# Kernel tuning notes

Hardware: AMD Instinct MI355X
Metric: run time of the kernel (lower is better)

## Reference

```python
import jax, jax.numpy as jnp
import numpy as np

FEATURE_IN = 4096
FEATURE_OUT = 4096
R = 16
ALPHA = 32.0


def setup_inputs() -> dict:
    key = jax.random.key(0)
    k_x, k_w, k_b, k_a = jax.random.split(key, 4)
    x = jax.random.normal(k_x, (4, 2048, FEATURE_IN), dtype=jnp.float32)
    # base linear (torch nn.Linear): weight [out, in], bias [out]
    bound = 1.0 / np.sqrt(FEATURE_IN)
    w = jax.random.uniform(k_w, (FEATURE_OUT, FEATURE_IN), dtype=jnp.float32, minval=-bound, maxval=bound)
    b = jax.random.uniform(k_b, (FEATURE_OUT,), dtype=jnp.float32, minval=-bound, maxval=bound)
    # lora_a: kaiming uniform over [feature_in, r]; lora_b: zeros -> use small randn so grads are nontrivial? No: faithful init is zeros, but zeros makes LoRA path trivially zero. Use kaiming for a, small random for b to exercise the math.
    gain = np.sqrt(2.0 / (1.0 + 5.0 ** 2))  # kaiming_uniform default a=sqrt(5)
    bound_a = gain * np.sqrt(3.0 / FEATURE_IN)
    lora_a = jax.random.uniform(k_a, (FEATURE_IN, R), dtype=jnp.float32, minval=-bound_a, maxval=bound_a)
    lora_b = jax.random.normal(jax.random.fold_in(key, 7), (R, FEATURE_OUT), dtype=jnp.float32) * 0.01
    return {"x": x, "w": w, "b": b, "lora_a": lora_a, "lora_b": lora_b}


def reference(x, w, b, lora_a, lora_b):
    # base linear: x @ W^T + b
    output1 = jnp.einsum('bsi,oi->bso', x, w) + b
    # faithful to source: materialize (A @ B) [feature_in, feature_out] first,
    # then x @ (A@B), scaled by alpha/r
    ab = jnp.matmul(lora_a, lora_b)  # [feature_in, feature_out]
    output2 = jnp.matmul(x, ab) * (ALPHA / R)
    return output2 + output1
```

## Files before the change

### kernel.cpp

```cpp
#include <hip/hip_runtime.h>
#include <cstdint>
#include <cstddef>

#define FEATURE_IN 4096
#define FEATURE_OUT 4096
#define RNK 16

typedef __bf16 bf16x8_t __attribute__((ext_vector_type(8)));
typedef __bf16 bf16x4_t __attribute__((ext_vector_type(4)));
typedef float f32x4_t __attribute__((ext_vector_type(4)));

#define FW_KB 128
#define FW_NB 32
#define NFUSE 4096
#define NCVTB 2048
#define CVT_THREADS (NCVTB * 256)
#define CVT_CHUNKS 16

__global__ __launch_bounds__(256) void prep_all(const float* __restrict__ x,
                                                uint16_t* __restrict__ xb,
                                                const float* __restrict__ w,
                                                const float* __restrict__ la,
                                                const float* __restrict__ lb,
                                                uint16_t* __restrict__ wf) {
    __shared__ float las[FW_KB * RNK];
    __shared__ float lbs[RNK * FW_NB];

    const int tid = threadIdx.x;

    if (blockIdx.x >= NFUSE) {
        const int tg = (blockIdx.x - NFUSE) * 256 + tid;
        const f32x4_t* xp = (const f32x4_t*)x;
        bf16x4_t* op = (bf16x4_t*)xb;
#pragma unroll
        for (int i = 0; i < CVT_CHUNKS; ++i) {
            const int idx = i * CVT_THREADS + tg;
            f32x4_t v = xp[idx];
            bf16x4_t o;
            o[0] = (__bf16)v[0]; o[1] = (__bf16)v[1];
            o[2] = (__bf16)v[2]; o[3] = (__bf16)v[3];
            op[idx] = o;
        }
        return;
    }

    const int bid = blockIdx.x;
    const int kb = (bid & 31) * FW_KB;
    const int nb = (bid >> 5) * FW_NB;

    {
        const float4* src = (const float4*)(la + (size_t)kb * RNK);
        float4* dst = (float4*)las;
        dst[tid] = src[tid];
        dst[tid + 256] = src[tid + 256];
    }
#pragma unroll
    for (int f = tid; f < RNK * FW_NB; f += 256) {
        int r = f >> 5;
        int nl = f & 31;
        lbs[r * FW_NB + nl] = lb[(size_t)r * FEATURE_OUT + nb + nl];
    }
    __syncthreads();

    const int nl = tid >> 3;
    const int kq = tid & 7;

    f32x4_t bcol[4];
#pragma unroll
    for (int r4 = 0; r4 < 4; ++r4) {
        f32x4_t v;
#pragma unroll
        for (int j = 0; j < 4; ++j) v[j] = lbs[(r4 * 4 + j) * FW_NB + nl];
        bcol[r4] = v;
    }

    const f32x4_t* las4 = (const f32x4_t*)las;
    const float* wrow = w + (size_t)(nb + nl) * FEATURE_IN + kb + kq * 16;
    uint16_t* wfrow = wf + (size_t)(nb + nl) * FEATURE_IN + kb + kq * 16;

#pragma unroll
    for (int h = 0; h < 2; ++h) {
        float4 wv0 = ((const float4*)wrow)[h * 2 + 0];
        float4 wv1 = ((const float4*)wrow)[h * 2 + 1];
        float wfv[8] = {wv0.x, wv0.y, wv0.z, wv0.w, wv1.x, wv1.y, wv1.z, wv1.w};
        bf16x8_t o;
#pragma unroll
        for (int j = 0; j < 8; ++j) {
            const int k = kq * 16 + h * 8 + j;
            float s = 0.f;
#pragma unroll
            for (int rr = 0; rr < 4; ++rr) {
                const int r4 = (rr + kq) & 3;
                f32x4_t av = las4[k * 4 + r4];
                f32x4_t bv = bcol[r4];
                s += av[0] * bv[0] + av[1] * bv[1] + av[2] * bv[2] + av[3] * bv[3];
            }
            o[j] = (__bf16)(wfv[j] + 2.f * s);
        }
        ((bf16x8_t*)wfrow)[h] = o;
    }
}

#define BM 256
#define BN 256
#define BK 32
#define NT (FEATURE_IN / BK)

#define ABUF(b) ((b) * 32768)
#define BBUF(b) ((b) * 32768 + 16384)

#define MFMA16X(S) do { _Pragma("unroll")                                                \
    for (int _mi = 0; _mi < 4; ++_mi) { _Pragma("unroll")                                \
        for (int _ni = 0; _ni < 4; ++_ni)                                                \
            acc[_mi][_ni] = __builtin_amdgcn_mfma_f32_16x16x32_bf16(                     \
                afx[S][_mi], bqr[S][_ni], acc[_mi][_ni], 0, 0, 0); } } while (0)

#define MFMA16Y(S) do { _Pragma("unroll")                                                \
    for (int _mi = 0; _mi < 4; ++_mi) { _Pragma("unroll")                                \
        for (int _ni = 0; _ni < 4; ++_ni)                                                \
            acc[4 + _mi][_ni] = __builtin_amdgcn_mfma_f32_16x16x32_bf16(                 \
                afy[_mi], bqr[S][_ni], acc[4 + _mi][_ni], 0, 0, 0); } } while (0)

#define READ_AFY(b) do { _Pragma("unroll")                                               \
    for (int _mi = 0; _mi < 4; ++_mi)                                                    \
        afy[_mi] = *(const bf16x8_t*)(lds + ABUF(b) + aoff[4 + _mi]); } while (0)

#define READ_R0(b, SN) do { _Pragma("unroll")                                            \
    for (int _mi = 0; _mi < 4; ++_mi)                                                    \
        afx[SN][_mi] = *(const bf16x8_t*)(lds + ABUF(b) + aoff[_mi]);                    \
    _Pragma("unroll")                                                                    \
    for (int _ni = 0; _ni < 4; ++_ni)                                                    \
        bqr[SN][_ni] = *(const bf16x8_t*)(lds + BBUF(b) + boff[_ni]); } while (0)

#define GLL(SRC, DSTOFF)                                                                 \
    __builtin_amdgcn_global_load_lds(                                                    \
        (const __attribute__((address_space(1))) void*)(SRC),                            \
        (__attribute__((address_space(3))) void*)(lds + (DSTOFF) + wv * 1024), 16, 0, 0)

#define STAGE_A(b) do { GLL(pA0, ABUF(b)); GLL(pA1, ABUF(b) + 8192);                     \
                        pA0 += BK; pA1 += BK; } while (0)
#define STAGE_B(b) do { GLL(pB0, BBUF(b)); GLL(pB1, BBUF(b) + 8192);                     \
                        pB0 += BK; pB1 += BK; } while (0)

#define PBAR() __builtin_amdgcn_s_barrier()
#define PRIO1 __builtin_amdgcn_s_setprio(1)
#define PRIO0 __builtin_amdgcn_s_setprio(0)
#define VMCNT(n) asm volatile("s_waitcnt vmcnt(" #n ")" ::: "memory")
#define SCHEDB() __builtin_amdgcn_sched_barrier(0)

#define TILE_BODY(CUR, NXT, S, SN)                                                       \
    READ_AFY(CUR);                                                                       \
    STAGE_A(NXT);                                                                        \
    SCHEDB();                                                                            \
    PRIO1; MFMA16X(S); PRIO0;                                                            \
    VMCNT(6);                                                                            \
    PBAR();                                                                              \
    READ_R0((CUR + 1) & 3, SN);                                                          \
    STAGE_B(NXT);                                                                        \
    SCHEDB();                                                                            \
    PRIO1; MFMA16Y(S); PRIO0;                                                            \
    PBAR();

#define TAIL_BODY(CUR, S, SN, NWAIT)                                                     \
    READ_AFY(CUR);                                                                       \
    SCHEDB();                                                                            \
    PRIO1; MFMA16X(S); PRIO0;                                                            \
    VMCNT(NWAIT);                                                                        \
    PBAR();                                                                              \
    READ_R0((CUR + 1) & 3, SN);                                                          \
    SCHEDB();                                                                            \
    PRIO1; MFMA16Y(S); PRIO0;                                                            \
    PBAR();

__global__ __launch_bounds__(512, 2) void gemm256(const uint16_t* __restrict__ Au,
                                                  const uint16_t* __restrict__ Bu,
                                                  const float* __restrict__ bias,
                                                  float* __restrict__ C,
                                                  int M, int N, int K) {
    __shared__ __align__(16) char lds[131072];

    const __bf16* A = (const __bf16*)Au;
    const __bf16* B = (const __bf16*)Bu;

    const int tid  = threadIdx.x;
    const int wv   = tid >> 6;
    const int lane = tid & 63;
    const int waveM = wv >> 2;
    const int waveN = wv & 3;
    const int l15 = lane & 15;
    const int q   = lane >> 4;

    const int nbx = N / BN;
    const int nwg = nbx * (M / BM);
    const int bidlin = blockIdx.y * nbx + blockIdx.x;
    const int swz = (bidlin & 7) * (nwg >> 3) + (bidlin >> 3);
    const int by = swz / nbx;
    const int bx = swz - by * nbx;
    const int m0 = by * BM;
    const int n0 = bx * BN;

    const int srow = tid >> 2;
    const int sq   = ((tid & 3) - (srow >> 1)) & 3;
    const __bf16* pA0 = A + (size_t)(m0 + srow) * K + sq * 8;
    const __bf16* pA1 = pA0 + (size_t)128 * K;
    const __bf16* pB0 = B + (size_t)(n0 + srow) * K + sq * 8;
    const __bf16* pB1 = pB0 + (size_t)128 * K;

    int aoff[8], boff[4];
#pragma unroll
    for (int mi = 0; mi < 8; ++mi) {
        int row = waveM * 128 + mi * 16 + l15;
        aoff[mi] = row * 64 + (((row >> 1) + q) & 3) * 16;
    }
#pragma unroll
    for (int ni = 0; ni < 4; ++ni) {
        int row = waveN * 64 + ni * 16 + l15;
        boff[ni] = row * 64 + (((row >> 1) + q) & 3) * 16;
    }

    f32x4_t acc[8][4];
#pragma unroll
    for (int mi = 0; mi < 8; ++mi)
#pragma unroll
        for (int ni = 0; ni < 4; ++ni)
            acc[mi][ni] = (f32x4_t)0.f;

    bf16x8_t afx[2][4], afy[4], bqr[2][4];

    STAGE_A(0); STAGE_B(0);
    STAGE_A(1); STAGE_B(1);
    STAGE_A(2); STAGE_B(2);
    VMCNT(8);
    PBAR();
    READ_R0(0, 0);

#pragma unroll 1
    for (int i = 0; i < 31; ++i) {
        TILE_BODY(0, 3, 0, 1)
        TILE_BODY(1, 0, 1, 0)
        TILE_BODY(2, 1, 0, 1)
        TILE_BODY(3, 2, 1, 0)
    }
    TILE_BODY(0, 3, 0, 1)

    TAIL_BODY(1, 1, 0, 4)
    TAIL_BODY(2, 0, 1, 0)
    READ_AFY(3);
    SCHEDB();
    PRIO1; MFMA16X(1); PRIO0;
    PRIO1; MFMA16Y(1); PRIO0;

#pragma unroll
    for (int ni = 0; ni < 4; ++ni) {
        const int col = n0 + waveN * 64 + ni * 16 + l15;
        const float bv = bias[col];
#pragma unroll
        for (int mi = 0; mi < 8; ++mi) {
            const int row = m0 + waveM * 128 + mi * 16 + q * 4;
            float* op = C + (size_t)row * N + col;
#pragma unroll
            for (int j = 0; j < 4; ++j)
                op[(size_t)j * N] = acc[mi][ni][j] + bv;
        }
    }
}

extern "C" void kernel_launch(void* const* d_in, const int* in_sizes, int n_in,
                              void* d_out, int out_size, void* d_ws, size_t ws_size,
                              hipStream_t stream) {
    const float* x  = (const float*)d_in[0];
    const float* w  = (const float*)d_in[1];
    const float* b  = (const float*)d_in[2];
    const float* la = (const float*)d_in[3];
    const float* lb = (const float*)d_in[4];
    float* out = (float*)d_out;

    const int M = in_sizes[0] / FEATURE_IN;
    const int K = FEATURE_IN;
    const int N = FEATURE_OUT;

    uint16_t* xb = (uint16_t*)d_ws;
    uint16_t* wf = (uint16_t*)((char*)d_ws + (size_t)M * K * 2);

    prep_all<<<NFUSE + NCVTB, 256, 0, stream>>>(x, xb, w, la, lb, wf);

    {
        dim3 grid(N / BN, M / BM);
        gemm256<<<grid, 512, 0, stream>>>(xb, wf, b, out, M, N, K);
    }
}
```

Before: 522.4 us.

## Restructure GEMM mainloop to BK=64 double-buffered half-tile 8-phase pipeline

Replaces the 4-stage BK=32 ring buffer with two BK=64 buffers split into A/B half-tiles, which are staged one at a time across eight phases per 128-wide K step. The wave-to-tile mapping changes: each wave covers 2 M-halves × 64 N-rows with reordered fragment reads and an XOR swizzle over 8 chunks. The aim is fewer barriers per K, larger contiguous global loads, and finer interleaving of LDS staging with MFMA. The cost is a shallower prefetch depth and more barrier points per phase, and the hand-written vmcnt accounting could stall or race.

```diff
diff --git a/kernel.cpp b/kernel.cpp
--- a/kernel.cpp
+++ b/kernel.cpp
@@ -103,80 +103,60 @@
 
 #define BM 256
 #define BN 256
-#define BK 32
-#define NT (FEATURE_IN / BK)
-
-#define ABUF(b) ((b) * 32768)
-#define BBUF(b) ((b) * 32768 + 16384)
-
-#define MFMA16X(S) do { _Pragma("unroll")                                                \
-    for (int _mi = 0; _mi < 4; ++_mi) { _Pragma("unroll")                                \
-        for (int _ni = 0; _ni < 4; ++_ni)                                                \
-            acc[_mi][_ni] = __builtin_amdgcn_mfma_f32_16x16x32_bf16(                     \
-                afx[S][_mi], bqr[S][_ni], acc[_mi][_ni], 0, 0, 0); } } while (0)
-
-#define MFMA16Y(S) do { _Pragma("unroll")                                                \
-    for (int _mi = 0; _mi < 4; ++_mi) { _Pragma("unroll")                                \
-        for (int _ni = 0; _ni < 4; ++_ni)                                                \
-            acc[4 + _mi][_ni] = __builtin_amdgcn_mfma_f32_16x16x32_bf16(                 \
-                afy[_mi], bqr[S][_ni], acc[4 + _mi][_ni], 0, 0, 0); } } while (0)
-
-#define READ_AFY(b) do { _Pragma("unroll")                                               \
-    for (int _mi = 0; _mi < 4; ++_mi)                                                    \
-        afy[_mi] = *(const bf16x8_t*)(lds + ABUF(b) + aoff[4 + _mi]); } while (0)
-
-#define READ_R0(b, SN) do { _Pragma("unroll")                                            \
-    for (int _mi = 0; _mi < 4; ++_mi)                                                    \
-        afx[SN][_mi] = *(const bf16x8_t*)(lds + ABUF(b) + aoff[_mi]);                    \
-    _Pragma("unroll")                                                                    \
-    for (int _ni = 0; _ni < 4; ++_ni)                                                    \
-        bqr[SN][_ni] = *(const bf16x8_t*)(lds + BBUF(b) + boff[_ni]); } while (0)
-
-#define GLL(SRC, DSTOFF)                                                                 \
+#define NPAIR 32
+
+#define AHT(b, h) ((b) * 65536 + (h) * 16384)
+#define BHT(b, h) ((b) * 65536 + 32768 + (h) * 16384)
+
+#define READ_A(BF, QD) do { _Pragma("unroll")                                            \
+    for (int _m = 0; _m < 2; ++_m) { _Pragma("unroll")                                   \
+        for (int _s = 0; _s < 2; ++_s)                                                   \
+            fa[_m][_s] = *(const bf16x8_t*)(lds + AHT(BF, waveM) +                       \
+                ((QD) * 2 + _m) * 2048 + aRow + ((_s) ? cs1 : cs0)); } } while (0)
+
+#define READ_B(BF) do { _Pragma("unroll")                                                \
+    for (int _n = 0; _n < 4; ++_n) { _Pragma("unroll")                                   \
+        for (int _s = 0; _s < 2; ++_s)                                                   \
+            fb[_n][_s] = *(const bf16x8_t*)(lds + BHT(BF, nHalf) +                       \
+                _n * 2048 + bRow + ((_s) ? cs1 : cs0)); } } while (0)
+
+#define MFMA16(QD) do { _Pragma("unroll")                                                \
+    for (int _s = 0; _s < 2; ++_s) { _Pragma("unroll")                                   \
+        for (int _m = 0; _m < 2; ++_m) { _Pragma("unroll")                               \
+            for (int _n = 0; _n < 4; ++_n)                                               \
+                acc[(QD) * 2 + _m][_n] = __builtin_amdgcn_mfma_f32_16x16x32_bf16(        \
+                    fa[_m][_s], fb[_n][_s], acc[(QD) * 2 + _m][_n], 0, 0, 0); } } } while (0)
+
+#define GLL(SRC, DST)                                                                    \
     __builtin_amdgcn_global_load_lds(                                                    \
         (const __attribute__((address_space(1))) void*)(SRC),                            \
-        (__attribute__((address_space(3))) void*)(lds + (DSTOFF) + wv * 1024), 16, 0, 0)
-
-#define STAGE_A(b) do { GLL(pA0, ABUF(b)); GLL(pA1, ABUF(b) + 8192);                     \
-                        pA0 += BK; pA1 += BK; } while (0)
-#define STAGE_B(b) do { GLL(pB0, BBUF(b)); GLL(pB1, BBUF(b) + 8192);                     \
-                        pB0 += BK; pB1 += BK; } while (0)
+        (__attribute__((address_space(3))) void*)(DST), 16, 0, 0)
+
+#define SA(BF, H, KO) do {                                                               \
+    GLL(((H) ? pA1 : pA0) + (KO),  lds + AHT(BF, H) + wv * 1024);                        \
+    GLL(((H) ? pA1b : pA0b) + (KO), lds + AHT(BF, H) + 8192 + wv * 1024); } while (0)
+#define SB(BF, H, KO) do {                                                               \
+    GLL(((H) ? pB1 : pB0) + (KO),  lds + BHT(BF, H) + wv * 1024);                        \
+    GLL(((H) ? pB1b : pB0b) + (KO), lds + BHT(BF, H) + 8192 + wv * 1024); } while (0)
 
 #define PBAR() __builtin_amdgcn_s_barrier()
 #define PRIO1 __builtin_amdgcn_s_setprio(1)
 #define PRIO0 __builtin_amdgcn_s_setprio(0)
 #define VMCNT(n) asm volatile("s_waitcnt vmcnt(" #n ")" ::: "memory")
+#define LGKM0() asm volatile("s_waitcnt lgkmcnt(0)" ::: "memory")
 #define SCHEDB() __builtin_amdgcn_sched_barrier(0)
 
-#define TILE_BODY(CUR, NXT, S, SN)                                                       \
-    READ_AFY(CUR);                                                                       \
-    STAGE_A(NXT);                                                                        \
+#define PH_TAIL(QD)                                                                      \
     SCHEDB();                                                                            \
-    PRIO1; MFMA16X(S); PRIO0;                                                            \
-    VMCNT(6);                                                                            \
     PBAR();                                                                              \
-    READ_R0((CUR + 1) & 3, SN);                                                          \
-    STAGE_B(NXT);                                                                        \
-    SCHEDB();                                                                            \
-    PRIO1; MFMA16Y(S); PRIO0;                                                            \
-    PBAR();
-
-#define TAIL_BODY(CUR, S, SN, NWAIT)                                                     \
-    READ_AFY(CUR);                                                                       \
-    SCHEDB();                                                                            \
-    PRIO1; MFMA16X(S); PRIO0;                                                            \
-    VMCNT(NWAIT);                                                                        \
-    PBAR();                                                                              \
-    READ_R0((CUR + 1) & 3, SN);                                                          \
-    SCHEDB();                                                                            \
-    PRIO1; MFMA16Y(S); PRIO0;                                                            \
-    PBAR();
-
-__global__ __launch_bounds__(512, 2) void gemm256(const uint16_t* __restrict__ Au,
-                                                  const uint16_t* __restrict__ Bu,
-                                                  const float* __restrict__ bias,
-                                                  float* __restrict__ C,
-                                                  int M, int N, int K) {
+    LGKM0(); SCHEDB();                                                                   \
+    PRIO1; MFMA16(QD); PRIO0;
+
+__global__ __launch_bounds__(512, 2) void gemm8p(const uint16_t* __restrict__ Au,
+                                                 const uint16_t* __restrict__ Bu,
+                                                 const float* __restrict__ bias,
+                                                 float* __restrict__ C,
+                                                 int M, int N, int K) {
     __shared__ __align__(16) char lds[131072];
 
     const __bf16* A = (const __bf16*)Au;
@@ -187,6 +167,7 @@
     const int lane = tid & 63;
     const int waveM = wv >> 2;
     const int waveN = wv & 3;
+    const int nHalf = waveN >> 1;
     const int l15 = lane & 15;
     const int q   = lane >> 4;
 
@@ -199,24 +180,22 @@
     const int m0 = by * BM;
     const int n0 = bx * BN;
 
-    const int srow = tid >> 2;
-    const int sq   = ((tid & 3) - (srow >> 1)) & 3;
-    const __bf16* pA0 = A + (size_t)(m0 + srow) * K + sq * 8;
-    const __bf16* pA1 = pA0 + (size_t)128 * K;
-    const __bf16* pB0 = B + (size_t)(n0 + srow) * K + sq * 8;
-    const __bf16* pB1 = pB0 + (size_t)128 * K;
-
-    int aoff[8], boff[4];
-#pragma unroll
-    for (int mi = 0; mi < 8; ++mi) {
-        int row = waveM * 128 + mi * 16 + l15;
-        aoff[mi] = row * 64 + (((row >> 1) + q) & 3) * 16;
-    }
-#pragma unroll
-    for (int ni = 0; ni < 4; ++ni) {
-        int row = waveN * 64 + ni * 16 + l15;
-        boff[ni] = row * 64 + (((row >> 1) + q) & 3) * 16;
-    }
+    const int srow = tid >> 3;
+    const int sc   = ((tid & 7) - (srow & 7)) & 7;
+    const __bf16* pA0  = A + (size_t)(m0 + srow) * K + sc * 8;
+    const __bf16* pA0b = pA0 + (size_t)64 * K;
+    const __bf16* pA1  = A + (size_t)(m0 + 128 + srow) * K + sc * 8;
+    const __bf16* pA1b = pA1 + (size_t)64 * K;
+    const __bf16* pB0  = B + (size_t)(n0 + srow) * K + sc * 8;
+    const __bf16* pB0b = pB0 + (size_t)64 * K;
+    const __bf16* pB1  = B + (size_t)(n0 + 128 + srow) * K + sc * 8;
+    const __bf16* pB1b = pB1 + (size_t)64 * K;
+
+    const int aRow = l15 * 128;
+    const int bRow = ((waveN & 1) * 64 + l15) * 128;
+    const int s0 = (q + (l15 & 7)) & 7;
+    const int cs0 = s0 * 16;
+    const int cs1 = (s0 ^ 4) * 16;
 
     f32x4_t acc[8][4];
 #pragma unroll
@@ -225,30 +204,79 @@
         for (int ni = 0; ni < 4; ++ni)
             acc[mi][ni] = (f32x4_t)0.f;
 
-    bf16x8_t afx[2][4], afy[4], bqr[2][4];
-
-    STAGE_A(0); STAGE_B(0);
-    STAGE_A(1); STAGE_B(1);
-    STAGE_A(2); STAGE_B(2);
-    VMCNT(8);
-    PBAR();
-    READ_R0(0, 0);
+    bf16x8_t fa[2][2], fb[4][2];
+
+    SA(0, 0, 0); SA(0, 1, 0); SB(0, 0, 0); SB(0, 1, 0);
+    SB(1, 0, 64); SB(1, 1, 64);
+    VMCNT(4);
+    PBAR();
 
 #pragma unroll 1
     for (int i = 0; i < 31; ++i) {
-        TILE_BODY(0, 3, 0, 1)
-        TILE_BODY(1, 0, 1, 0)
-        TILE_BODY(2, 1, 0, 1)
-        TILE_BODY(3, 2, 1, 0)
-    }
-    TILE_BODY(0, 3, 0, 1)
-
-    TAIL_BODY(1, 1, 0, 4)
-    TAIL_BODY(2, 0, 1, 0)
-    READ_AFY(3);
+        READ_A(0, 0); READ_B(0);
+        SA(1, 0, 64); SA(1, 1, 64);
+        PH_TAIL(0);
+        PBAR();
+        READ_A(0, 1);
+        SB(0, 0, 128);
+        PH_TAIL(1);
+        PBAR();
+        READ_A(0, 2);
+        SB(0, 1, 128);
+        PH_TAIL(2);
+        PBAR();
+        READ_A(0, 3);
+        PH_TAIL(3);
+        VMCNT(4);
+        PBAR();
+        READ_A(1, 0); READ_B(1);
+        SA(0, 0, 128);
+        PH_TAIL(0);
+        PBAR();
+        READ_A(1, 1);
+        SA(0, 1, 128);
+        PH_TAIL(1);
+        PBAR();
+        READ_A(1, 2);
+        SB(1, 0, 192);
+        PH_TAIL(2);
+        PBAR();
+        READ_A(1, 3);
+        SB(1, 1, 192);
+        PH_TAIL(3);
+        VMCNT(4);
+        PBAR();
+        pA0 += 128; pA0b += 128; pA1 += 128; pA1b += 128;
+        pB0 += 128; pB0b += 128; pB1 += 128; pB1b += 128;
+    }
+
+    READ_A(0, 0); READ_B(0);
+    SA(1, 0, 64); SA(1, 1, 64);
+    PH_TAIL(0);
+    PBAR();
+    READ_A(0, 1);
+    PH_TAIL(1);
+    PBAR();
+    READ_A(0, 2);
+    PH_TAIL(2);
+    PBAR();
+    READ_A(0, 3);
+    PH_TAIL(3);
+    VMCNT(0);
+    PBAR();
+    READ_A(1, 0); READ_B(1);
+    PH_TAIL(0);
+    PBAR();
+    READ_A(1, 1);
+    PH_TAIL(1);
+    PBAR();
+    READ_A(1, 2);
+    PH_TAIL(2);
+    PBAR();
+    READ_A(1, 3);
     SCHEDB();
-    PRIO1; MFMA16X(1); PRIO0;
-    PRIO1; MFMA16Y(1); PRIO0;
+    LGKM0(); SCHEDB();
+    PRIO1; MFMA16(3); PRIO0;
 
 #pragma unroll
     for (int ni = 0; ni < 4; ++ni) {
@@ -286,6 +314,6 @@
 
     {
         dim3 grid(N / BN, M / BM);
-        gemm256<<<grid, 512, 0, stream>>>(xb, wf, b, out, M, N, K);
+        gemm8p<<<grid, 512, 0, stream>>>(xb, wf, b, out, M, N, K);
     }
 }
```

New measurement: 504.9 us. -3.3%, faster.
